# Kernel optimization log

Hardware: AMD Instinct MI355X
Metric: run time of the kernel (lower is better)

The kernel has to match this reference:

```python
import jax, jax.numpy as jnp
import numpy as np

N, F, H = 4096, 256, 4

def setup_inputs() -> dict:
    key = jax.random.key(0)
    kx, kw, kb = jax.random.split(key, 3)
    x = jax.random.normal(kx, (N, F), dtype=jnp.float32)
    # per-head Linear(2F -> 1): weight [H, 2F], bias [H]
    lim = 1.0 / np.sqrt(2 * F)
    W = jax.random.uniform(kw, (H, 2 * F), minval=-lim, maxval=lim, dtype=jnp.float32)
    b = jax.random.uniform(kb, (H,), minval=-lim, maxval=lim, dtype=jnp.float32)
    return {"x": x, "W": W, "b": b}

def reference(x, W, b):
    n, f = x.shape
    # concat(x_i, x_j) @ w^T == x_i @ w1 + x_j @ w2  (separable score, same math)
    W1, W2 = W[:, :f], W[:, f:]            # [H,F] each
    s_i = x @ W1.T                          # [N,H] contribution of row node i
    s_j = x @ W2.T                          # [N,H] contribution of col node j
    # logits[h,i,j] = s_i[i,h] + s_j[j,h] + b[h]
    logits = s_i.T[:, :, None] + s_j.T[:, None, :] + b[:, None, None]  # [H,N,N]
    attn = jax.nn.softmax(logits, axis=2)   # softmax over neighbors j
    out_heads = jnp.einsum('hij,jf->hif', attn, x)  # [H,N,F]
    avg = jnp.mean(out_heads, axis=0)       # [N,F]
    return jax.nn.leaky_relu(avg, negative_slope=0.2)
```

## Files before the change

kernel.cpp:

```cpp
#include <hip/hip_runtime.h>


#define NROWS 4096
#define FDIM  256
#define HH    4
#define RPB   32
#define NB1   (NROWS / RPB)
#define PADF  260
#define RPB2  32
#define NB2   (NROWS / RPB2)


__global__ __launch_bounds__(256) void k1_part(const float* __restrict__ x,
                                               const float* __restrict__ W,
                                               float* __restrict__ u_part,
                                               float* __restrict__ z_part) {
    __shared__ __align__(16) float x_lds[RPB * PADF];
    __shared__ __align__(16) float w_lds[HH * PADF];
    __shared__ __align__(16) float e_lds[RPB * HH];

    const int t = threadIdx.x;
    const int b = blockIdx.x;
    const int row0 = b * RPB;

    {
        int h = t >> 6, c4 = t & 63;
        float4 wv = ((const float4*)W)[(size_t)h * (2 * FDIM / 4) + (FDIM / 4) + c4];
        *(float4*)&w_lds[h * PADF + c4 * 4] = wv;
    }
    for (int i = t; i < RPB * (FDIM / 4); i += 256) {
        int r = i >> 6, c4 = i & 63;
        float4 v = ((const float4*)x)[(size_t)(row0 + r) * (FDIM / 4) + c4];
        *(float4*)&x_lds[r * PADF + c4 * 4] = v;
    }
    __syncthreads();

    {
        int r = t >> 3, h = (t >> 1) & 3, half = t & 1;
        const float4* xr = (const float4*)&x_lds[r * PADF];
        const float4* wr = (const float4*)&w_lds[h * PADF];
        float acc = 0.f;
        #pragma unroll
        for (int i = 0; i < 32; ++i) {
            float4 a = xr[half * 32 + i];
            float4 w = wr[half * 32 + i];
            acc = fmaf(a.x, w.x, acc); acc = fmaf(a.y, w.y, acc);
            acc = fmaf(a.z, w.z, acc); acc = fmaf(a.w, w.w, acc);
        }
        acc += __shfl_xor(acc, 1);
        if (half == 0) e_lds[r * 4 + h] = __expf(acc);
    }
    __syncthreads();

    if (t < HH) {
        float z = 0.f;
        #pragma unroll
        for (int r = 0; r < RPB; ++r) z += e_lds[r * 4 + t];
        z_part[b * HH + t] = z;
    }

    float a0 = 0.f, a1 = 0.f, a2 = 0.f, a3 = 0.f;
    #pragma unroll 8
    for (int r = 0; r < RPB; ++r) {
        float xv = x_lds[r * PADF + t];
        float4 e4 = *(const float4*)&e_lds[r * 4];
        a0 = fmaf(e4.x, xv, a0);
        a1 = fmaf(e4.y, xv, a1);
        a2 = fmaf(e4.z, xv, a2);
        a3 = fmaf(e4.w, xv, a3);
    }
    float* up = u_part + (size_t)b * (HH * FDIM);
    up[0 * FDIM + t] = a0;
    up[1 * FDIM + t] = a1;
    up[2 * FDIM + t] = a2;
    up[3 * FDIM + t] = a3;
}

__global__ __launch_bounds__(256) void k2_out(const float* __restrict__ u_part,
                                              const float* __restrict__ z_part,
                                              float* __restrict__ out) {
    __shared__ __align__(16) float v_lds[FDIM];
    __shared__ float z_lds[NB1 * HH];
    __shared__ float z_fin[HH];
    const int t = threadIdx.x;

    z_lds[t]       = z_part[t];
    z_lds[t + 256] = z_part[t + 256];
    __syncthreads();
    if (t < HH) {
        float z = 0.f;
        for (int bb = 0; bb < NB1; ++bb) z += z_lds[bb * 4 + t];
        z_fin[t] = z;
    }

    float a0 = 0.f, a1 = 0.f, a2 = 0.f, a3 = 0.f;
    for (int bb = 0; bb < NB1; ++bb) {
        const float* up = u_part + (size_t)bb * (HH * FDIM);
        a0 += up[0 * FDIM + t];
        a1 += up[1 * FDIM + t];
        a2 += up[2 * FDIM + t];
        a3 += up[3 * FDIM + t];
    }
    __syncthreads();
    float val = 0.25f * (a0 / z_fin[0] + a1 / z_fin[1] + a2 / z_fin[2] + a3 / z_fin[3]);
    v_lds[t] = val > 0.f ? val : 0.2f * val;
    __syncthreads();

    const int row0 = blockIdx.x * RPB2;
    const int c4 = t & 63;
    const int sub = t >> 6;
    float4 v4 = *(const float4*)&v_lds[c4 * 4];
    float4* out4 = (float4*)out;
    #pragma unroll
    for (int k = 0; k < RPB2 / 4; ++k)
        out4[(size_t)(row0 + sub * (RPB2 / 4) + k) * (FDIM / 4) + c4] = v4;
}

extern "C" void kernel_launch(void* const* d_in, const int* in_sizes, int n_in,
                              void* d_out, int out_size, void* d_ws, size_t ws_size,
                              hipStream_t stream) {
    const float* x = (const float*)d_in[0];
    const float* W = (const float*)d_in[1];
    float* u_part = (float*)d_ws;
    float* z_part = u_part + (size_t)NB1 * HH * FDIM;
    float* out = (float*)d_out;

    k1_part<<<NB1, 256, 0, stream>>>(x, W, u_part, z_part);
    k2_out<<<NB2, 256, 0, stream>>>(u_part, z_part, out);
}
```

Measured before the change: 70.86 us.

## Fuse partial-reduction and broadcast kernels via cooperative grid sync

Merges the two kernels into a single cooperative launch. Each block computes its partial weighted sums, then waits at a grid-wide sync before reducing all partials and writing its slice of the output. The aim is to remove the second launch and the gap between the kernels. In exchange it pays for a grid barrier and depends on all 128 blocks being resident at once. It also reuses the x tile in shared memory for the second phase.

```diff
diff --git a/kernel.cpp b/kernel.cpp
--- a/kernel.cpp
+++ b/kernel.cpp
@@ -1,20 +1,22 @@
 #include <hip/hip_runtime.h>
+#include <hip/hip_cooperative_groups.h>
+
+namespace cg = cooperative_groups;
 
 
 #define NROWS 4096
 #define FDIM  256
 #define HH    4
 #define RPB   32
-#define NB1   (NROWS / RPB)
+#define NB    (NROWS / RPB)
 #define PADF  260
-#define RPB2  32
-#define NB2   (NROWS / RPB2)
 
 
-__global__ __launch_bounds__(256) void k1_part(const float* __restrict__ x,
+__global__ __launch_bounds__(256) void k_fused(const float* __restrict__ x,
                                                const float* __restrict__ W,
                                                float* __restrict__ u_part,
-                                               float* __restrict__ z_part) {
+                                               float* __restrict__ z_part,
+                                               float* __restrict__ out) {
     __shared__ __align__(16) float x_lds[RPB * PADF];
     __shared__ __align__(16) float w_lds[HH * PADF];
     __shared__ __align__(16) float e_lds[RPB * HH];
@@ -22,6 +24,7 @@
     const int t = threadIdx.x;
     const int b = blockIdx.x;
     const int row0 = b * RPB;
+
 
     {
         int h = t >> 6, c4 = t & 63;
@@ -59,42 +62,42 @@
         z_part[b * HH + t] = z;
     }
 
-    float a0 = 0.f, a1 = 0.f, a2 = 0.f, a3 = 0.f;
-    #pragma unroll 8
-    for (int r = 0; r < RPB; ++r) {
-        float xv = x_lds[r * PADF + t];
-        float4 e4 = *(const float4*)&e_lds[r * 4];
-        a0 = fmaf(e4.x, xv, a0);
-        a1 = fmaf(e4.y, xv, a1);
-        a2 = fmaf(e4.z, xv, a2);
-        a3 = fmaf(e4.w, xv, a3);
+    {
+        float a0 = 0.f, a1 = 0.f, a2 = 0.f, a3 = 0.f;
+        #pragma unroll 8
+        for (int r = 0; r < RPB; ++r) {
+            float xv = x_lds[r * PADF + t];
+            float4 e4 = *(const float4*)&e_lds[r * 4];
+            a0 = fmaf(e4.x, xv, a0);
+            a1 = fmaf(e4.y, xv, a1);
+            a2 = fmaf(e4.z, xv, a2);
+            a3 = fmaf(e4.w, xv, a3);
+        }
+        float* up = u_part + (size_t)b * (HH * FDIM);
+        up[0 * FDIM + t] = a0;
+        up[1 * FDIM + t] = a1;
+        up[2 * FDIM + t] = a2;
+        up[3 * FDIM + t] = a3;
     }
-    float* up = u_part + (size_t)b * (HH * FDIM);
-    up[0 * FDIM + t] = a0;
-    up[1 * FDIM + t] = a1;
-    up[2 * FDIM + t] = a2;
-    up[3 * FDIM + t] = a3;
-}
 
-__global__ __launch_bounds__(256) void k2_out(const float* __restrict__ u_part,
-                                              const float* __restrict__ z_part,
-                                              float* __restrict__ out) {
-    __shared__ __align__(16) float v_lds[FDIM];
-    __shared__ float z_lds[NB1 * HH];
-    __shared__ float z_fin[HH];
-    const int t = threadIdx.x;
+    __threadfence();
+    cg::this_grid().sync();
 
-    z_lds[t]       = z_part[t];
-    z_lds[t + 256] = z_part[t + 256];
+    float* v_lds = x_lds;
+    float* zl    = x_lds + FDIM;
+    float* zf    = x_lds + FDIM + NB * HH;
+
+    zl[t]       = z_part[t];
+    zl[t + 256] = z_part[t + 256];
     __syncthreads();
     if (t < HH) {
         float z = 0.f;
-        for (int bb = 0; bb < NB1; ++bb) z += z_lds[bb * 4 + t];
-        z_fin[t] = z;
+        for (int bb = 0; bb < NB; ++bb) z += zl[bb * 4 + t];
+        zf[t] = z;
     }
 
     float a0 = 0.f, a1 = 0.f, a2 = 0.f, a3 = 0.f;
-    for (int bb = 0; bb < NB1; ++bb) {
+    for (int bb = 0; bb < NB; ++bb) {
         const float* up = u_part + (size_t)bb * (HH * FDIM);
         a0 += up[0 * FDIM + t];
         a1 += up[1 * FDIM + t];
@@ -102,18 +105,17 @@
         a3 += up[3 * FDIM + t];
     }
     __syncthreads();
-    float val = 0.25f * (a0 / z_fin[0] + a1 / z_fin[1] + a2 / z_fin[2] + a3 / z_fin[3]);
+    float val = 0.25f * (a0 / zf[0] + a1 / zf[1] + a2 / zf[2] + a3 / zf[3]);
     v_lds[t] = val > 0.f ? val : 0.2f * val;
     __syncthreads();
 
-    const int row0 = blockIdx.x * RPB2;
     const int c4 = t & 63;
     const int sub = t >> 6;
     float4 v4 = *(const float4*)&v_lds[c4 * 4];
     float4* out4 = (float4*)out;
     #pragma unroll
-    for (int k = 0; k < RPB2 / 4; ++k)
-        out4[(size_t)(row0 + sub * (RPB2 / 4) + k) * (FDIM / 4) + c4] = v4;
+    for (int k = 0; k < RPB / 4; ++k)
+        out4[(size_t)(row0 + sub * (RPB / 4) + k) * (FDIM / 4) + c4] = v4;
 }
 
 extern "C" void kernel_launch(void* const* d_in, const int* in_sizes, int n_in,
@@ -122,9 +124,10 @@
     const float* x = (const float*)d_in[0];
     const float* W = (const float*)d_in[1];
     float* u_part = (float*)d_ws;
-    float* z_part = u_part + (size_t)NB1 * HH * FDIM;
+    float* z_part = u_part + (size_t)NB * HH * FDIM;
     float* out = (float*)d_out;
 
-    k1_part<<<NB1, 256, 0, stream>>>(x, W, u_part, z_part);
-    k2_out<<<NB2, 256, 0, stream>>>(u_part, z_part, out);
+    void* args[] = { (void*)&x, (void*)&W, (void*)&u_part, (void*)&z_part, (void*)&out };
+    hipLaunchCooperativeKernel(reinterpret_cast<void*>(k_fused),
+                               dim3(NB), dim3(256), args, 0, stream);
 }
```

Result: slower. 109.3 us (+54.2%).

## Halve k1 rows per block and split k2 reduction across column slices

Applied to the files above, without the earlier changes.

k1 now processes 16 rows per block, doubling the block count to 256, and splits each dot product four ways with a rotated LDS index to spread bank accesses. k2 previously had every block redundantly reduce all partial sums. Now each block owns a 16-column slice and a range of output rows, reduces only that slice using float4 loads across 16 segments, and writes 256 rows. This removes the redundant full reduction in every k2 block, in exchange for more partials for k2 to read and extra LDS reduction stages.

```diff
diff --git a/kernel.cpp b/kernel.cpp
--- a/kernel.cpp
+++ b/kernel.cpp
@@ -4,11 +4,15 @@
 #define NROWS 4096
 #define FDIM  256
 #define HH    4
-#define RPB   32
+
+#define RPB   16
 #define NB1   (NROWS / RPB)
 #define PADF  260
-#define RPB2  32
-#define NB2   (NROWS / RPB2)
+
+#define NCS   16
+#define CSW   (FDIM / NCS)
+#define NRR   16
+#define RPB2  (NROWS / NRR)
 
 
 __global__ __launch_bounds__(256) void k1_part(const float* __restrict__ x,
@@ -25,30 +29,32 @@
 
     {
         int h = t >> 6, c4 = t & 63;
-        float4 wv = ((const float4*)W)[(size_t)h * (2 * FDIM / 4) + (FDIM / 4) + c4];
+        float4 wv = ((const float4*)W)[(size_t)h * 128 + 64 + c4];
         *(float4*)&w_lds[h * PADF + c4 * 4] = wv;
     }
-    for (int i = t; i < RPB * (FDIM / 4); i += 256) {
+    for (int i = t; i < RPB * 64; i += 256) {
         int r = i >> 6, c4 = i & 63;
-        float4 v = ((const float4*)x)[(size_t)(row0 + r) * (FDIM / 4) + c4];
+        float4 v = ((const float4*)x)[(size_t)(row0 + r) * 64 + c4];
         *(float4*)&x_lds[r * PADF + c4 * 4] = v;
     }
     __syncthreads();
 
     {
-        int r = t >> 3, h = (t >> 1) & 3, half = t & 1;
+        int r = t >> 4, h = (t >> 2) & 3, q = t & 3;
         const float4* xr = (const float4*)&x_lds[r * PADF];
         const float4* wr = (const float4*)&w_lds[h * PADF];
         float acc = 0.f;
         #pragma unroll
-        for (int i = 0; i < 32; ++i) {
-            float4 a = xr[half * 32 + i];
-            float4 w = wr[half * 32 + i];
+        for (int i = 0; i < 16; ++i) {
+            int idx = q * 16 + ((i + q * 4) & 15);
+            float4 a = xr[idx];
+            float4 w = wr[idx];
             acc = fmaf(a.x, w.x, acc); acc = fmaf(a.y, w.y, acc);
             acc = fmaf(a.z, w.z, acc); acc = fmaf(a.w, w.w, acc);
         }
         acc += __shfl_xor(acc, 1);
-        if (half == 0) e_lds[r * 4 + h] = __expf(acc);
+        acc += __shfl_xor(acc, 2);
+        if (q == 0) e_lds[r * 4 + h] = __expf(acc);
     }
     __syncthreads();
 
@@ -59,61 +65,89 @@
         z_part[b * HH + t] = z;
     }
 
-    float a0 = 0.f, a1 = 0.f, a2 = 0.f, a3 = 0.f;
-    #pragma unroll 8
-    for (int r = 0; r < RPB; ++r) {
-        float xv = x_lds[r * PADF + t];
-        float4 e4 = *(const float4*)&e_lds[r * 4];
-        a0 = fmaf(e4.x, xv, a0);
-        a1 = fmaf(e4.y, xv, a1);
-        a2 = fmaf(e4.z, xv, a2);
-        a3 = fmaf(e4.w, xv, a3);
+    {
+        float a0 = 0.f, a1 = 0.f, a2 = 0.f, a3 = 0.f;
+        #pragma unroll
+        for (int r = 0; r < RPB; ++r) {
+            float xv = x_lds[r * PADF + t];
+            float4 e4 = *(const float4*)&e_lds[r * 4];
+            a0 = fmaf(e4.x, xv, a0);
+            a1 = fmaf(e4.y, xv, a1);
+            a2 = fmaf(e4.z, xv, a2);
+            a3 = fmaf(e4.w, xv, a3);
+        }
+        float* up = u_part + (size_t)b * (HH * FDIM);
+        up[0 * FDIM + t] = a0;
+        up[1 * FDIM + t] = a1;
+        up[2 * FDIM + t] = a2;
+        up[3 * FDIM + t] = a3;
     }
-    float* up = u_part + (size_t)b * (HH * FDIM);
-    up[0 * FDIM + t] = a0;
-    up[1 * FDIM + t] = a1;
-    up[2 * FDIM + t] = a2;
-    up[3 * FDIM + t] = a3;
 }
 
 __global__ __launch_bounds__(256) void k2_out(const float* __restrict__ u_part,
                                               const float* __restrict__ z_part,
                                               float* __restrict__ out) {
-    __shared__ __align__(16) float v_lds[FDIM];
-    __shared__ float z_lds[NB1 * HH];
-    __shared__ float z_fin[HH];
+    __shared__ __align__(16) float red[16][HH][CSW];
+    __shared__ float red2[HH][CSW];
+    __shared__ float zq[16][HH];
+    __shared__ float zf[HH];
+    __shared__ __align__(16) float v_lds[CSW];
+
     const int t = threadIdx.x;
+    const int cs = blockIdx.x & (NCS - 1);
+    const int rr = blockIdx.x >> 4;
 
-    z_lds[t]       = z_part[t];
-    z_lds[t + 256] = z_part[t + 256];
+    if (t < 64) {
+        int h = t & 3, seg = t >> 2;
+        float z = 0.f;
+        #pragma unroll 4
+        for (int pb = seg * 16; pb < seg * 16 + 16; ++pb)
+            z += z_part[pb * HH + h];
+        zq[seg][h] = z;
+    }
+
+    {
+        int f4c = t & 3, h = (t >> 2) & 3, seg = t >> 4;
+        const float4* base = (const float4*)u_part + (size_t)h * (FDIM / 4) + cs * 4 + f4c;
+        float4 a = {0.f, 0.f, 0.f, 0.f};
+        #pragma unroll 4
+        for (int pb = seg * 16; pb < seg * 16 + 16; ++pb) {
+            float4 u4 = base[(size_t)pb * (HH * FDIM / 4)];
+            a.x += u4.x; a.y += u4.y; a.z += u4.z; a.w += u4.w;
+        }
+        *(float4*)&red[seg][h][f4c * 4] = a;
+    }
     __syncthreads();
     if (t < HH) {
         float z = 0.f;
-        for (int bb = 0; bb < NB1; ++bb) z += z_lds[bb * 4 + t];
-        z_fin[t] = z;
-    }
-
-    float a0 = 0.f, a1 = 0.f, a2 = 0.f, a3 = 0.f;
-    for (int bb = 0; bb < NB1; ++bb) {
-        const float* up = u_part + (size_t)bb * (HH * FDIM);
-        a0 += up[0 * FDIM + t];
-        a1 += up[1 * FDIM + t];
-        a2 += up[2 * FDIM + t];
-        a3 += up[3 * FDIM + t];
+        #pragma unroll
+        for (int s = 0; s < 16; ++s) z += zq[s][t];
+        zf[t] = z;
     }
     __syncthreads();
-    float val = 0.25f * (a0 / z_fin[0] + a1 / z_fin[1] + a2 / z_fin[2] + a3 / z_fin[3]);
-    v_lds[t] = val > 0.f ? val : 0.2f * val;
+    if (t < 64) {
+        int h = t >> 4, col = t & 15;
+        float a = 0.f;
+        #pragma unroll
+        for (int s = 0; s < 16; ++s) a += red[s][h][col];
+        red2[h][col] = a / zf[h];
+    }
+    __syncthreads();
+    if (t < CSW) {
+        float v = 0.25f * (red2[0][t] + red2[1][t] + red2[2][t] + red2[3][t]);
+        v_lds[t] = v > 0.f ? v : 0.2f * v;
+    }
     __syncthreads();
 
-    const int row0 = blockIdx.x * RPB2;
-    const int c4 = t & 63;
-    const int sub = t >> 6;
-    float4 v4 = *(const float4*)&v_lds[c4 * 4];
+    const int f4c = t & 3;
+    const int rbase = rr * RPB2;
+    float4 v4 = *(const float4*)&v_lds[f4c * 4];
     float4* out4 = (float4*)out;
     #pragma unroll
-    for (int k = 0; k < RPB2 / 4; ++k)
-        out4[(size_t)(row0 + sub * (RPB2 / 4) + k) * (FDIM / 4) + c4] = v4;
+    for (int p = 0; p < 4; ++p) {
+        int row = rbase + p * 64 + (t >> 2);
+        out4[(size_t)row * (FDIM / 4) + cs * 4 + f4c] = v4;
+    }
 }
 
 extern "C" void kernel_launch(void* const* d_in, const int* in_sizes, int n_in,
@@ -126,5 +160,5 @@
     float* out = (float*)d_out;
 
     k1_part<<<NB1, 256, 0, stream>>>(x, W, u_part, z_part);
-    k2_out<<<NB2, 256, 0, stream>>>(u_part, z_part, out);
+    k2_out<<<NCS * NRR, 256, 0, stream>>>(u_part, z_part, out);
 }
```

New measurement: 65.23 us (median of 2 runs). 1.09x faster.
